# Kernel tuning notes

Hardware: AMD Instinct MI355X
Metric: run time of the kernel (lower is better)

## Reference

```python
import jax, jax.numpy as jnp
import numpy as np

M, D, H, E = 4096, 2048, 2048, 8


def q8(t):
    # Emulate fp8 e4m3 quantize->dequantize (DeepGEMM inputs); scale is all-ones in the source.
    return t.astype(jnp.float8_e4m3fn).astype(jnp.float32)


def setup_inputs() -> dict:
    key = jax.random.key(0)
    k1, k2, k3 = jax.random.split(key, 3)
    x = jax.random.normal(k1, (M, D), dtype=jnp.float32)
    gate_w = jax.random.normal(k2, (E, D), dtype=jnp.float32) * (D ** -0.5)
    gate_b = jnp.zeros((E,), dtype=jnp.float32)
    expert_w = jax.random.normal(k3, (E, H, D), dtype=jnp.float32) * (D ** -0.5)
    return {"x": x, "gate_w": gate_w, "gate_b": gate_b, "expert_w": expert_w}


def reference(x, gate_w, gate_b, expert_w):
    # Gating: softmax over experts. [M, E]
    gate_scores = jax.nn.softmax(x @ gate_w.T + gate_b, axis=-1)
    # fp8 quantize-dequantize of activations and expert weights (rhs_scale == 1).
    x_q = q8(x)                      # [M, D]
    w_q = q8(expert_w)               # [E, H, D]
    # Grouped GEMM (every expert applied to every token), bf16 output like deep_gemm.
    y = jnp.einsum("md,ehd->emh", x_q, w_q).astype(jnp.bfloat16)  # [E, M, H]
    # Weighted combine: sum_e gate[m,e] * y[e,m,h]
    out = jnp.einsum("me,emh->mh", gate_scores, y.astype(jnp.float32))  # [M, H]
    return out
```

## Files before the change

### kernel.cpp

```cpp
#include <hip/hip_runtime.h>
#include <hip/hip_bf16.h>

#define MDIM 4096
#define DDIM 2048
#define HDIM 2048
#define EDIM 8
#define HD   ((size_t)HDIM * DDIM)

typedef float v4f __attribute__((ext_vector_type(4)));
typedef int   v4i __attribute__((ext_vector_type(4)));
typedef int   v8i __attribute__((ext_vector_type(8)));

__device__ __forceinline__ void gl2lds16(const void* g, void* l) {
  __builtin_amdgcn_global_load_lds(
      (const __attribute__((address_space(1))) void*)g,
      (__attribute__((address_space(3))) void*)l,
      16, 0, 0);
}

__global__ __launch_bounds__(256) void k_gate_xq(
    const float* __restrict__ x, const float* __restrict__ gw,
    const float* __restrict__ gb, float* __restrict__ gate,
    unsigned char* __restrict__ x8)
{
  const int wid  = threadIdx.x >> 6;
  const int lane = threadIdx.x & 63;
  const int m    = blockIdx.x * 4 + wid;

  const float4* xr = (const float4*)(x + (size_t)m * DDIM);
  unsigned int* qr = (unsigned int*)(x8 + (size_t)m * DDIM);

  float part[EDIM];
#pragma unroll
  for (int e = 0; e < EDIM; ++e) part[e] = 0.f;

#pragma unroll
  for (int it = 0; it < DDIM / 4 / 64; ++it) {
    const int idx = it * 64 + lane;
    const float4 xv = xr[idx];
    int pk = __builtin_amdgcn_cvt_pk_fp8_f32(xv.x, xv.y, 0, false);
    pk = __builtin_amdgcn_cvt_pk_fp8_f32(xv.z, xv.w, pk, true);
    qr[idx] = (unsigned int)pk;
#pragma unroll
    for (int e = 0; e < EDIM; ++e) {
      const float4 wv = ((const float4*)(gw + (size_t)e * DDIM))[idx];
      part[e] += xv.x * wv.x + xv.y * wv.y + xv.z * wv.z + xv.w * wv.w;
    }
  }
#pragma unroll
  for (int e = 0; e < EDIM; ++e) {
#pragma unroll
    for (int off = 32; off > 0; off >>= 1)
      part[e] += __shfl_xor(part[e], off);
  }
  float lg[EDIM];
  float s = 0.f;
#pragma unroll
  for (int e = 0; e < EDIM; ++e) lg[e] = part[e] + gb[e];
  float mx = lg[0];
#pragma unroll
  for (int e = 1; e < EDIM; ++e) mx = fmaxf(mx, lg[e]);
#pragma unroll
  for (int e = 0; e < EDIM; ++e) { lg[e] = expf(lg[e] - mx); s += lg[e]; }
  const float inv = 1.f / s;
  if (lane < EDIM) gate[m * EDIM + lane] = lg[lane] * inv;
}

__global__ void k_wq(const float* __restrict__ w, unsigned char* __restrict__ w8)
{
  const long long n4 = (long long)EDIM * HDIM * DDIM / 4;
  const long long stride = (long long)gridDim.x * blockDim.x;
  for (long long i = (long long)blockIdx.x * blockDim.x + threadIdx.x; i < n4;
       i += stride) {
    const float4 v = ((const float4*)w)[i];
    int pk = __builtin_amdgcn_cvt_pk_fp8_f32(v.x, v.y, 0, false);
    pk = __builtin_amdgcn_cvt_pk_fp8_f32(v.z, v.w, pk, true);
    ((unsigned int*)w8)[i] = (unsigned int)pk;
  }
}

__global__ __launch_bounds__(256, 2) void k_moe_gemm(
    const unsigned char* __restrict__ x8,
    const unsigned char* __restrict__ w8,
    const float* __restrict__ gate,
    float* __restrict__ out)
{
  extern __shared__ unsigned char smem[];

  const int tid  = threadIdx.x;
  const int lane = tid & 63;
  const int wid  = tid >> 6;
  const int wm   = wid >> 1;
  const int wn   = wid & 1;

  const int bid   = blockIdx.x;
  const int xcd   = bid & 7;
  const int local = bid >> 3;
  const int tm    = (xcd >> 1) * 8 + (local >> 3);
  const int tn    = (xcd & 1) * 8 + (local & 7);
  const int bm    = tm * 128;
  const int bn    = tn * 128;

  const int lrow = lane & 15;
  const int lk   = lane >> 4;
  const int c0   = (lk * 32) ^ ((lrow & 7) << 4);
  const int c1   = c0 ^ 16;

  const int strow = tid >> 3;
  const int stcol = ((tid & 7) * 16) ^ ((strow & 7) << 4);
  const unsigned char* asrc = x8 + (size_t)(bm + strow) * DDIM + stcol;
  const unsigned char* bsrc = w8 + (size_t)(bn + strow) * DDIM + stcol;

  float* sGf = (float*)(smem + 65536);

  if (tid < 128) {
    const float4 g0 = *(const float4*)(gate + (size_t)(bm + tid) * EDIM);
    const float4 g1 = *(const float4*)(gate + (size_t)(bm + tid) * EDIM + 4);
    sGf[0 * 128 + tid] = g0.x; sGf[1 * 128 + tid] = g0.y;
    sGf[2 * 128 + tid] = g0.z; sGf[3 * 128 + tid] = g0.w;
    sGf[4 * 128 + tid] = g1.x; sGf[5 * 128 + tid] = g1.y;
    sGf[6 * 128 + tid] = g1.z; sGf[7 * 128 + tid] = g1.w;
  }

  v4f acc[4][4];
  v4f outacc[4][4];
#pragma unroll
  for (int i = 0; i < 4; ++i)
#pragma unroll
    for (int j = 0; j < 4; ++j) {
      acc[i][j][0] = 0.f; acc[i][j][1] = 0.f;
      acc[i][j][2] = 0.f; acc[i][j][3] = 0.f;
      outacc[i][j][0] = 0.f; outacc[i][j][1] = 0.f;
      outacc[i][j][2] = 0.f; outacc[i][j][3] = 0.f;
    }

#define STAGE(S) do {                                                          \
    const int    kb_ = ((S) & 15) * 128;                                       \
    const size_t eo_ = (size_t)((S) >> 4) * HD;                                \
    unsigned char* la_ = smem + ((S) & 1) * 16384;                             \
    unsigned char* lb_ = smem + 32768 + ((S) & 1) * 16384;                     \
    _Pragma("unroll") for (int i = 0; i < 4; ++i)                              \
      gl2lds16(asrc + (size_t)i * (32 * DDIM) + kb_,                           \
               (void*)(la_ + i * 4096 + wid * 1024));                          \
    _Pragma("unroll") for (int i = 0; i < 4; ++i)                              \
      gl2lds16(bsrc + eo_ + (size_t)i * (32 * DDIM) + kb_,                     \
               (void*)(lb_ + i * 4096 + wid * 1024));                          \
  } while (0)

#define COMP(S) do {                                                           \
    const unsigned char* pA_ = smem + ((S) & 1) * 16384 +                      \
                               (size_t)(wm * 64 + lrow) * 128;                 \
    const unsigned char* pB_ = smem + 32768 + ((S) & 1) * 16384 +              \
                               (size_t)(wn * 64 + lrow) * 128;                 \
    v8i bv_[4];                                                                \
    _Pragma("unroll") for (int j = 0; j < 4; ++j) {                            \
      union { v8i v; v4i h[2]; } u_;                                           \
      u_.h[0] = *(const v4i*)(pB_ + j * 2048 + c0);                            \
      u_.h[1] = *(const v4i*)(pB_ + j * 2048 + c1);                            \
      bv_[j] = u_.v;                                                           \
    }                                                                          \
    __builtin_amdgcn_s_setprio(1);                                             \
    _Pragma("unroll") for (int i = 0; i < 4; ++i) {                            \
      union { v8i v; v4i h[2]; } ua_;                                          \
      ua_.h[0] = *(const v4i*)(pA_ + i * 2048 + c0);                           \
      ua_.h[1] = *(const v4i*)(pA_ + i * 2048 + c1);                           \
      const v8i av_ = ua_.v;                                                   \
      _Pragma("unroll") for (int j = 0; j < 4; ++j)                            \
        acc[i][j] = __builtin_amdgcn_mfma_scale_f32_16x16x128_f8f6f4(          \
            av_, bv_[j], acc[i][j], 0 , 0 ,                      \
            0, 127 , 0, 127 );                         \
    }                                                                          \
    __builtin_amdgcn_s_setprio(0);                                             \
    if (((S) & 15) == 15) {         \
      const int e_ = (S) >> 4;                                                 \
      _Pragma("unroll") for (int i = 0; i < 4; ++i) {                          \
        const v4f g4_ =                                                        \
            *(const v4f*)(sGf + e_ * 128 + wm * 64 + i * 16 + lk * 4);         \
        _Pragma("unroll") for (int j = 0; j < 4; ++j) {                        \
          outacc[i][j][0] += g4_[0] * acc[i][j][0]; acc[i][j][0] = 0.f;        \
          outacc[i][j][1] += g4_[1] * acc[i][j][1]; acc[i][j][1] = 0.f;        \
          outacc[i][j][2] += g4_[2] * acc[i][j][2]; acc[i][j][2] = 0.f;        \
          outacc[i][j][3] += g4_[3] * acc[i][j][3]; acc[i][j][3] = 0.f;        \
        }                                                                      \
      }                                                                        \
    }                                                                          \
  } while (0)

  STAGE(0);
  __syncthreads();

  for (int s = 0; s < 127; ++s) {
    STAGE(s + 1);
    asm volatile("s_waitcnt vmcnt(8)" ::: "memory");
    __builtin_amdgcn_s_barrier();
    __builtin_amdgcn_sched_barrier(0);
    COMP(s);
    __builtin_amdgcn_s_barrier();
  }
  asm volatile("s_waitcnt vmcnt(0)" ::: "memory");
  __builtin_amdgcn_s_barrier();
  COMP(127);

#undef COMP
#undef STAGE

#pragma unroll
  for (int i = 0; i < 4; ++i)
#pragma unroll
    for (int q = 0; q < 4; ++q) {
      const size_t r = (size_t)(bm + wm * 64 + i * 16 + lk * 4 + q);
      float* orow = out + r * HDIM + bn + wn * 64 + lrow;
#pragma unroll
      for (int j = 0; j < 4; ++j)
        orow[j * 16] = outacc[i][j][q];
    }
}

extern "C" void kernel_launch(void* const* d_in, const int* in_sizes, int n_in,
                              void* d_out, int out_size, void* d_ws, size_t ws_size,
                              hipStream_t stream) {
  (void)in_sizes; (void)n_in; (void)out_size; (void)ws_size;
  const float* x        = (const float*)d_in[0];
  const float* gate_w   = (const float*)d_in[1];
  const float* gate_b   = (const float*)d_in[2];
  const float* expert_w = (const float*)d_in[3];
  float* out = (float*)d_out;

  char* ws = (char*)d_ws;
  float* gate       = (float*)ws;
  unsigned char* x8 = (unsigned char*)(ws + 131072);
  unsigned char* w8 = (unsigned char*)(ws + 131072 + (size_t)MDIM * DDIM);

  hipLaunchKernelGGL(k_gate_xq, dim3(MDIM / 4), dim3(256), 0, stream,
                     x, gate_w, gate_b, gate, x8);
  hipLaunchKernelGGL(k_wq, dim3(4096), dim3(256), 0, stream, expert_w, w8);
  hipLaunchKernelGGL(k_moe_gemm, dim3(512), dim3(256), 69632, stream,
                     x8, w8, gate, out);
}
```

Measured before the change: 166.9 us.

## Load expert-weight operand directly into registers with double buffering, bypassing LDS

The B (expert weight) tiles are now read straight from global memory into per-wave registers, ping-ponged across two register sets, instead of being staged through LDS. Only the activation tile still goes through LDS. This halves shared memory per block, which may allow more blocks per CU, and merges the per-stage barriers into one. In exchange, waves that share the same B columns now fetch them from global memory redundantly, and register pressure goes up.

```diff
diff --git a/kernel.cpp b/kernel.cpp
--- a/kernel.cpp
+++ b/kernel.cpp
@@ -109,9 +109,11 @@
   const int strow = tid >> 3;
   const int stcol = ((tid & 7) * 16) ^ ((strow & 7) << 4);
   const unsigned char* asrc = x8 + (size_t)(bm + strow) * DDIM + stcol;
-  const unsigned char* bsrc = w8 + (size_t)(bn + strow) * DDIM + stcol;
-
-  float* sGf = (float*)(smem + 65536);
+
+  const unsigned char* bptr =
+      w8 + (size_t)(bn + wn * 64 + lrow) * DDIM + lk * 32;
+
+  float* sGf = (float*)(smem + 32768);
 
   if (tid < 128) {
     const float4 g0 = *(const float4*)(gate + (size_t)(bm + tid) * EDIM);
@@ -134,42 +136,53 @@
       outacc[i][j][2] = 0.f; outacc[i][j][3] = 0.f;
     }
 
-#define STAGE(S) do {                                                          \
-    const int    kb_ = ((S) & 15) * 128;                                       \
-    const size_t eo_ = (size_t)((S) >> 4) * HD;                                \
+  v8i bvA[4], bvB[4];
+
+#define STAGE_A(S) do {                                                        \
+    const int kb_ = ((S) & 15) * 128;                                          \
     unsigned char* la_ = smem + ((S) & 1) * 16384;                             \
-    unsigned char* lb_ = smem + 32768 + ((S) & 1) * 16384;                     \
     _Pragma("unroll") for (int i = 0; i < 4; ++i)                              \
       gl2lds16(asrc + (size_t)i * (32 * DDIM) + kb_,                           \
                (void*)(la_ + i * 4096 + wid * 1024));                          \
-    _Pragma("unroll") for (int i = 0; i < 4; ++i)                              \
-      gl2lds16(bsrc + eo_ + (size_t)i * (32 * DDIM) + kb_,                     \
-               (void*)(lb_ + i * 4096 + wid * 1024));                          \
   } while (0)
 
-#define COMP(S) do {                                                           \
-    const unsigned char* pA_ = smem + ((S) & 1) * 16384 +                      \
-                               (size_t)(wm * 64 + lrow) * 128;                 \
-    const unsigned char* pB_ = smem + 32768 + ((S) & 1) * 16384 +              \
-                               (size_t)(wn * 64 + lrow) * 128;                 \
-    v8i bv_[4];                                                                \
+#define LOAD_B(S, BV) do {                                                     \
+    const unsigned char* pbe_ = bptr + (size_t)((S) >> 4) * HD +               \
+                                (size_t)(((S) & 15) * 128);                    \
     _Pragma("unroll") for (int j = 0; j < 4; ++j) {                            \
+      const unsigned char* pb_ = pbe_ + (size_t)j * (16 * DDIM);               \
       union { v8i v; v4i h[2]; } u_;                                           \
-      u_.h[0] = *(const v4i*)(pB_ + j * 2048 + c0);                            \
-      u_.h[1] = *(const v4i*)(pB_ + j * 2048 + c1);                            \
-      bv_[j] = u_.v;                                                           \
+      u_.h[0] = *(const v4i*)(pb_);                                            \
+      u_.h[1] = *(const v4i*)(pb_ + 16);                                       \
+      BV[j] = u_.v;                                                            \
+    }                                                                          \
+  } while (0)
+
+#define BODY(S, BVC, BVN) do {                                                 \
+    asm volatile("s_waitcnt vmcnt(8)" ::: "memory");            \
+    __builtin_amdgcn_s_barrier();                                              \
+    if ((S) < 127) {                                                           \
+      STAGE_A((S) + 1);                                                        \
+      asm volatile("" ::: "memory");       \
+      LOAD_B((S) + 1, BVN);                                                    \
+    }                                                                          \
+    v8i av[4];                                                                 \
+    {                                                                          \
+      const unsigned char* pA_ = smem + ((S) & 1) * 16384 +                    \
+                                 (size_t)(wm * 64 + lrow) * 128;               \
+      _Pragma("unroll") for (int f = 0; f < 4; ++f) {                          \
+        union { v8i v; v4i h[2]; } u_;                                         \
+        u_.h[0] = *(const v4i*)(pA_ + f * 2048 + c0);                          \
+        u_.h[1] = *(const v4i*)(pA_ + f * 2048 + c1);                          \
+        av[f] = u_.v;                                                          \
+      }                                                                        \
     }                                                                          \
     __builtin_amdgcn_s_setprio(1);                                             \
-    _Pragma("unroll") for (int i = 0; i < 4; ++i) {                            \
-      union { v8i v; v4i h[2]; } ua_;                                          \
-      ua_.h[0] = *(const v4i*)(pA_ + i * 2048 + c0);                           \
-      ua_.h[1] = *(const v4i*)(pA_ + i * 2048 + c1);                           \
-      const v8i av_ = ua_.v;                                                   \
-      _Pragma("unroll") for (int j = 0; j < 4; ++j)                            \
+    _Pragma("unroll") for (int j = 0; j < 4; ++j)                              \
+      _Pragma("unroll") for (int i = 0; i < 4; ++i)                            \
         acc[i][j] = __builtin_amdgcn_mfma_scale_f32_16x16x128_f8f6f4(          \
-            av_, bv_[j], acc[i][j], 0 , 0 ,                      \
+            av[i], BVC[j], acc[i][j], 0 , 0 ,                    \
             0, 127 , 0, 127 );                         \
-    }                                                                          \
     __builtin_amdgcn_s_setprio(0);                                             \
     if (((S) & 15) == 15) {         \
       const int e_ = (S) >> 4;                                                 \
@@ -186,23 +199,18 @@
     }                                                                          \
   } while (0)
 
-  STAGE(0);
+  STAGE_A(0);
+  LOAD_B(0, bvA);
   __syncthreads();
 
-  for (int s = 0; s < 127; ++s) {
-    STAGE(s + 1);
-    asm volatile("s_waitcnt vmcnt(8)" ::: "memory");
-    __builtin_amdgcn_s_barrier();
-    __builtin_amdgcn_sched_barrier(0);
-    COMP(s);
-    __builtin_amdgcn_s_barrier();
-  }
-  asm volatile("s_waitcnt vmcnt(0)" ::: "memory");
-  __builtin_amdgcn_s_barrier();
-  COMP(127);
-
-#undef COMP
-#undef STAGE
+  for (int s = 0; s < 128; s += 2) {
+    BODY(s,     bvA, bvB);
+    BODY(s + 1, bvB, bvA);
+  }
+
+#undef BODY
+#undef LOAD_B
+#undef STAGE_A
 
 #pragma unroll
   for (int i = 0; i < 4; ++i)
@@ -234,6 +242,6 @@
   hipLaunchKernelGGL(k_gate_xq, dim3(MDIM / 4), dim3(256), 0, stream,
                      x, gate_w, gate_b, gate, x8);
   hipLaunchKernelGGL(k_wq, dim3(4096), dim3(256), 0, stream, expert_w, w8);
-  hipLaunchKernelGGL(k_moe_gemm, dim3(512), dim3(256), 69632, stream,
+  hipLaunchKernelGGL(k_moe_gemm, dim3(512), dim3(256), 36864, stream,
                      x8, w8, gate, out);
 }
```

Measured after the change: 358.0 us. 114% more time.
